# Optimization experiments

Measured on AMD Instinct MI355X. Metric: run time of the kernel, lower is better.

Reference implementation:

```python
import jax, jax.numpy as jnp
import numpy as np

N_NODES = 100000
N_EDGES = 3200000
IN_CH = 256
HIDDEN = 64
OUT_CH = 128


def setup_inputs() -> dict:
    key = jax.random.key(0)
    ks = jax.random.split(key, 6)
    x = jax.random.normal(ks[0], (N_NODES, IN_CH), dtype=jnp.float32)
    edge_index = jax.random.randint(ks[1], (2, N_EDGES), 0, N_NODES, dtype=jnp.int64)
    W1 = jax.random.normal(ks[2], (IN_CH, HIDDEN), dtype=jnp.float32) * (1.0 / np.sqrt(IN_CH))
    b1 = jnp.zeros((HIDDEN,), dtype=jnp.float32)
    W2 = jax.random.normal(ks[3], (HIDDEN, OUT_CH), dtype=jnp.float32) * (1.0 / np.sqrt(HIDDEN))
    b2 = jnp.zeros((OUT_CH,), dtype=jnp.float32)
    fcW = jax.random.normal(ks[4], (2, OUT_CH), dtype=jnp.float32) * (1.0 / np.sqrt(OUT_CH))
    fcb = jnp.zeros((2,), dtype=jnp.float32)
    return {"x": x, "edge_index": edge_index, "W1": W1, "b1": b1,
            "W2": W2, "b2": b2, "fcW": fcW, "fcb": fcb}


def _gcn_conv(x, edge_index, W, b):
    """PyG GCNConv: linear transform, add self-loops, symmetric D^-1/2 A D^-1/2 aggregation, bias."""
    N = x.shape[0]
    h = x @ W  # [N, F_out]
    loops = jnp.arange(N, dtype=edge_index.dtype)
    row = jnp.concatenate([edge_index[0], loops])  # source nodes
    col = jnp.concatenate([edge_index[1], loops])  # destination nodes
    deg = jax.ops.segment_sum(jnp.ones_like(col, dtype=h.dtype), col, num_segments=N)
    dinv = jnp.where(deg > 0, jax.lax.rsqrt(deg), 0.0)
    norm = dinv[row] * dinv[col]  # [E+N]
    out = jax.ops.segment_sum(h[row] * norm[:, None], col, num_segments=N)
    return out + b


def reference(x, edge_index, W1, b1, W2, b2, fcW, fcb):
    h = jax.nn.relu(_gcn_conv(x, edge_index, W1, b1))
    h = jax.nn.relu(_gcn_conv(h, edge_index, W2, b2))
    g = jnp.mean(h, axis=0)  # [OUT_CH]
    return g @ fcW.T + fcb   # [2]
```

## Files before the change

kernel.cpp:

```cpp
#include <hip/hip_runtime.h>

#define N_NODES 100000
#define N_EDGES 3200000
#define C_IN 256
#define C_H 64
#define C_OUT 128
#define NB 391
#define G2F 625
#define NTILES 6250
#define CH1 8192

typedef unsigned int u32;
typedef unsigned short u16;
typedef unsigned long long u64;
typedef __attribute__((ext_vector_type(8))) short bf16x8;
typedef __attribute__((ext_vector_type(4))) float f32x4;

__device__ __forceinline__ float bflo(u32 p) {
    union { u32 i; float f; } v; v.i = p << 16; return v.f;
}
__device__ __forceinline__ float bfhi(u32 p) {
    union { u32 i; float f; } v; v.i = p & 0xffff0000u; return v.f;
}
__device__ __forceinline__ float bf2f(u16 u) {
    union { u32 i; float f; } v; v.i = ((u32)u) << 16; return v.f;
}
__device__ __forceinline__ u16 f2bf(float f) {
    union { float f; u32 i; } v; v.f = f;
    u32 x = v.i;
    return (u16)((x + 0x7fffu + ((x >> 16) & 1u)) >> 16);
}

__global__ void k_detect(const void* __restrict__ x, const void* __restrict__ ei,
                         const void* __restrict__ b1, const void* __restrict__ b2,
                         const void* __restrict__ fcW, const void* __restrict__ fcb,
                         int* __restrict__ flags,
                         float* __restrict__ b1c, float* __restrict__ b2c,
                         float* __restrict__ fcWc, float* __restrict__ fcbc) {
    __shared__ int sf[2];
    int t = threadIdx.x;
    if (t < 64) {
        u32 w = ((const u32*)x)[t];
        u32 low = w & 0xffffu;
        int e = (int)((low >> 7) & 0xff);
        bool inw = (e > 96 && e < 160) || (low == 0);
        u64 m = __ballot(inw);
        if (t == 0) sf[0] = (__popcll(m) >= 60) ? 1 : 0;
    } else if (t < 128) {
        int i = t - 64;
        u32 w = ((const u32*)ei)[2 * i + 1];
        u64 m = __ballot(w == 0);
        if (i == 0) sf[1] = (m == ~0ull) ? 1 : 0;
    }
    __syncthreads();
    if (t == 0) { flags[0] = sf[0]; flags[1] = sf[1]; }
    int isbf = sf[0];
    if (isbf) {
        const u16* p1 = (const u16*)b1;  const u16* p2 = (const u16*)b2;
        const u16* pw = (const u16*)fcW; const u16* pb = (const u16*)fcb;
        for (int i = t; i < C_H; i += 256) b1c[i] = bf2f(p1[i]);
        for (int i = t; i < C_OUT; i += 256) b2c[i] = bf2f(p2[i]);
        for (int i = t; i < 2 * C_OUT; i += 256) fcWc[i] = bf2f(pw[i]);
        for (int i = t; i < 2; i += 256) fcbc[i] = bf2f(pb[i]);
    } else {
        const float* p1 = (const float*)b1;  const float* p2 = (const float*)b2;
        const float* pw = (const float*)fcW; const float* pb = (const float*)fcb;
        for (int i = t; i < C_H; i += 256) b1c[i] = p1[i];
        for (int i = t; i < C_OUT; i += 256) b2c[i] = p2[i];
        for (int i = t; i < 2 * C_OUT; i += 256) fcWc[i] = pw[i];
        for (int i = t; i < 2; i += 256) fcbc[i] = pb[i];
    }
}

__global__ __launch_bounds__(256) void k_prep(const void* __restrict__ W1,
                                              const void* __restrict__ W2,
                                              const int* __restrict__ flags,
                                              u16* __restrict__ W1m, u16* __restrict__ W2m,
                                              u32* __restrict__ bucket_cnt) {
    int b = blockIdx.x, t = threadIdx.x;
    int isbf = flags[0];
    int i = b * 256 + t;
    if (i < NB) bucket_cnt[i] = 0;
    if (i < C_IN * C_H) {
        const u16* w1b = (const u16*)W1; const float* w1f = (const float*)W1;
        int j = i & 7, lane = (i >> 3) & 63, nt = (i >> 9) & 3, k0 = i >> 11;
        int k = k0 * 32 + ((lane >> 4) & 3) * 8 + j;
        int n = nt * 16 + (lane & 15);
        W1m[i] = isbf ? w1b[k * C_H + n] : f2bf(w1f[k * C_H + n]);
    } else {
        int i2 = i - C_IN * C_H;
        const u16* w2b = (const u16*)W2; const float* w2f = (const float*)W2;
        int j = i2 & 7, lane = (i2 >> 3) & 63, nt = (i2 >> 9) & 7, k0 = (i2 >> 12) & 1;
        int k = k0 * 32 + ((lane >> 4) & 3) * 8 + j;
        int n = nt * 16 + (lane & 15);
        W2m[i2] = isbf ? w2b[k * C_OUT + n] : f2bf(w2f[k * C_OUT + n]);
    }
}

__global__ __launch_bounds__(256) void k_hist1(const int* __restrict__ ei,
                                               const int* __restrict__ flags,
                                               u32* __restrict__ bucket_cnt) {
    __shared__ u32 h[NB];
    int t = threadIdx.x;
    int is64 = flags[1];
    for (int i = t; i < NB; i += 256) h[i] = 0;
    __syncthreads();
    int e0 = blockIdx.x * CH1;
    int nv = min(CH1, N_EDGES - e0);
    for (int i = t; i < nv; i += 256) {
        int e = e0 + i;
        int d = is64 ? ei[2 * (N_EDGES + e)] : ei[N_EDGES + e];
        atomicAdd(&h[d >> 8], 1u);
    }
    __syncthreads();
    for (int i = t; i < NB; i += 256)
        if (h[i]) atomicAdd(&bucket_cnt[i], h[i]);
}

__global__ __launch_bounds__(512) void k_bscan(const u32* __restrict__ bucket_cnt,
                                               u32* __restrict__ bucket_base,
                                               u32* __restrict__ bucket_cursor,
                                               int* __restrict__ rowptr) {
    __shared__ u32 sm[512];
    int t = threadIdx.x;
    u32 v = (t < NB) ? bucket_cnt[t] : 0;
    sm[t] = v;
    __syncthreads();
    for (int off = 1; off < 512; off <<= 1) {
        u32 a = (t >= off) ? sm[t - off] : 0;
        __syncthreads();
        sm[t] += a;
        __syncthreads();
    }
    if (t < NB) {
        u32 excl = sm[t] - v;
        bucket_base[t] = excl;
        bucket_cursor[t] = excl;
    }
    if (t == 0) {
        bucket_base[NB] = N_EDGES;
        rowptr[N_NODES] = N_EDGES;
    }
}

__global__ __launch_bounds__(512) void k_scatter1(const int* __restrict__ ei,
                                                  const int* __restrict__ flags,
                                                  u32* __restrict__ bucket_cursor,
                                                  u32* __restrict__ ebuf) {
    __shared__ u32 cnt[NB];
    __shared__ u32 lcur[NB];
    __shared__ u32 gbase[NB];
    __shared__ u32 lofs[512];
    __shared__ u32 stp[CH1];
    __shared__ u16 stb[CH1];
    int t = threadIdx.x;
    int is64 = flags[1];
    int e0 = blockIdx.x * CH1;
    int nv = min(CH1, N_EDGES - e0);
    for (int i = t; i < NB; i += 512) { cnt[i] = 0; lcur[i] = 0; }
    __syncthreads();
    for (int i = t; i < nv; i += 512) {
        int e = e0 + i;
        int d = is64 ? ei[2 * (N_EDGES + e)] : ei[N_EDGES + e];
        atomicAdd(&cnt[d >> 8], 1u);
    }
    __syncthreads();
    u32 v = (t < NB) ? cnt[t] : 0;
    lofs[t] = v;
    __syncthreads();
    for (int off = 1; off < 512; off <<= 1) {
        u32 a = (t >= off) ? lofs[t - off] : 0;
        __syncthreads();
        lofs[t] += a;
        __syncthreads();
    }
    u32 excl = lofs[t] - v;
    __syncthreads();
    lofs[t] = excl;
    __syncthreads();
    for (int i = t; i < nv; i += 512) {
        int e = e0 + i;
        int d, s;
        if (is64) { d = ei[2 * (N_EDGES + e)]; s = ei[2 * e]; }
        else      { d = ei[N_EDGES + e];       s = ei[e]; }
        int b = d >> 8;
        u32 slot = lofs[b] + atomicAdd(&lcur[b], 1u);
        stp[slot] = ((u32)(d & 255) << 20) | (u32)s;
        stb[slot] = (u16)b;
    }
    __syncthreads();
    for (int b = t; b < NB; b += 512) {
        u32 c = cnt[b];
        gbase[b] = c ? atomicAdd(&bucket_cursor[b], c) : 0;
    }
    __syncthreads();
    for (int s = t; s < nv; s += 512) {
        int b = stb[s];
        ebuf[gbase[b] + (s - lofs[b])] = stp[s];
    }
}

__global__ __launch_bounds__(256) void k_scatter2(const u32* __restrict__ bucket_base,
                                                  const u32* __restrict__ ebuf,
                                                  int* __restrict__ rowptr,
                                                  float* __restrict__ dinv,
                                                  int* __restrict__ csr) {
    __shared__ int cnt[256];
    __shared__ int pfx[256];
    __shared__ int lcur[256];
    int b = blockIdx.x, t = threadIdx.x;
    int ebeg = (int)bucket_base[b], eend = (int)bucket_base[b + 1];
    cnt[t] = 0;
    lcur[t] = 0;
    __syncthreads();
    for (int i = ebeg + t; i < eend; i += 256)
        atomicAdd(&cnt[(ebuf[i] >> 20) & 255], 1);
    __syncthreads();
    int v = cnt[t];
    pfx[t] = v;
    __syncthreads();
    for (int off = 1; off < 256; off <<= 1) {
        int a = (t >= off) ? pfx[t - off] : 0;
        __syncthreads();
        pfx[t] += a;
        __syncthreads();
    }
    int node = (b << 8) + t;
    if (node < N_NODES) {
        rowptr[node] = ebeg + (pfx[t] - v);
        dinv[node] = rsqrtf((float)(v + 1));
    }
    __syncthreads();
    for (int i = ebeg + t; i < eend; i += 256) {
        u32 p = ebuf[i];
        int dl = (p >> 20) & 255;
        int pos = ebeg + (pfx[dl] - cnt[dl]) + atomicAdd(&lcur[dl], 1);
        csr[pos] = (int)(p & 0x1FFFFu);
    }
}

__global__ __launch_bounds__(256) void k_gemm1(const void* __restrict__ xv,
                                               const u16* __restrict__ W1m,
                                               const float* __restrict__ dinv,
                                               u16* __restrict__ g1,
                                               const int* __restrict__ flags) {
    __shared__ u16 wlds[C_IN * C_H];
    int t = threadIdx.x;
    int isbf = flags[0];
    {
        const uint4* src = (const uint4*)W1m;
        uint4* dst = (uint4*)wlds;
#pragma unroll
        for (int it = 0; it < 8; ++it) dst[t + it * 256] = src[t + it * 256];
    }
    __syncthreads();
    int w = t >> 6, lane = t & 63;
    int quad = lane >> 4, mrow = lane & 15;
    int m0 = blockIdx.x * 128 + w * 32;
    if (m0 >= N_NODES) return;

    bf16x8 a[2][8];
    if (isbf) {
        const u16* xb = (const u16*)xv;
#pragma unroll
        for (int mt = 0; mt < 2; ++mt)
#pragma unroll
            for (int k0 = 0; k0 < 8; ++k0)
                a[mt][k0] = *(const bf16x8*)(xb + (size_t)(m0 + mt * 16 + mrow) * C_IN + k0 * 32 + quad * 8);
    } else {
        const float* xf = (const float*)xv;
#pragma unroll
        for (int mt = 0; mt < 2; ++mt)
#pragma unroll
            for (int k0 = 0; k0 < 8; ++k0) {
                const float* p = xf + (size_t)(m0 + mt * 16 + mrow) * C_IN + k0 * 32 + quad * 8;
                float4 v0 = *(const float4*)p;
                float4 v1 = *(const float4*)(p + 4);
                bf16x8 r;
                r[0] = (short)f2bf(v0.x); r[1] = (short)f2bf(v0.y);
                r[2] = (short)f2bf(v0.z); r[3] = (short)f2bf(v0.w);
                r[4] = (short)f2bf(v1.x); r[5] = (short)f2bf(v1.y);
                r[6] = (short)f2bf(v1.z); r[7] = (short)f2bf(v1.w);
                a[mt][k0] = r;
            }
    }

    float dv0[4], dv1[4];
#pragma unroll
    for (int r = 0; r < 4; ++r) {
        dv0[r] = dinv[m0 + quad * 4 + r];
        dv1[r] = dinv[m0 + 16 + quad * 4 + r];
    }

#pragma unroll
    for (int nt = 0; nt < 4; ++nt) {
        bf16x8 b[8];
#pragma unroll
        for (int k0 = 0; k0 < 8; ++k0)
            b[k0] = *(const bf16x8*)&wlds[((k0 * 4 + nt) * 64 + lane) * 8];
        f32x4 acc0 = {0.f, 0.f, 0.f, 0.f};
        f32x4 acc1 = {0.f, 0.f, 0.f, 0.f};
#pragma unroll
        for (int k0 = 0; k0 < 8; ++k0) {
            acc0 = __builtin_amdgcn_mfma_f32_16x16x32_bf16(a[0][k0], b[k0], acc0, 0, 0, 0);
            acc1 = __builtin_amdgcn_mfma_f32_16x16x32_bf16(a[1][k0], b[k0], acc1, 0, 0, 0);
        }
        int ch = nt * 16 + mrow;
#pragma unroll
        for (int r = 0; r < 4; ++r) {
            g1[(size_t)(m0 + quad * 4 + r) * C_H + ch] = f2bf(acc0[r] * dv0[r]);
            g1[(size_t)(m0 + 16 + quad * 4 + r) * C_H + ch] = f2bf(acc1[r] * dv1[r]);
        }
    }
}

template <int MODE>
__global__ __launch_bounds__(256) void k_gatherT(const int* __restrict__ rowptr,
                                                 const int* __restrict__ csr_src,
                                                 const float* __restrict__ dinv,
                                                 const u16* __restrict__ g,
                                                 const float* __restrict__ bias,
                                                 u16* __restrict__ out) {
    int t = threadIdx.x;
    int w = t >> 6, lane = t & 63;
    int grp = lane >> 3, c = lane & 7;
    int n = blockIdx.x * 4 + w;
    int beg = rowptr[n], end = rowptr[n + 1];
    float acc[8] = {0.f, 0.f, 0.f, 0.f, 0.f, 0.f, 0.f, 0.f};
    int e = beg + grp;
    for (; e + 8 < end; e += 16) {
        int sa = csr_src[e];
        int sb = csr_src[e + 8];
        uint4 pa = *(const uint4*)(g + (size_t)sa * C_H + c * 8);
        uint4 pb = *(const uint4*)(g + (size_t)sb * C_H + c * 8);
        acc[0] += bflo(pa.x); acc[1] += bfhi(pa.x);
        acc[2] += bflo(pa.y); acc[3] += bfhi(pa.y);
        acc[4] += bflo(pa.z); acc[5] += bfhi(pa.z);
        acc[6] += bflo(pa.w); acc[7] += bfhi(pa.w);
        acc[0] += bflo(pb.x); acc[1] += bfhi(pb.x);
        acc[2] += bflo(pb.y); acc[3] += bfhi(pb.y);
        acc[4] += bflo(pb.z); acc[5] += bfhi(pb.z);
        acc[6] += bflo(pb.w); acc[7] += bfhi(pb.w);
    }
    if (e < end) {
        int sa = csr_src[e];
        uint4 pa = *(const uint4*)(g + (size_t)sa * C_H + c * 8);
        acc[0] += bflo(pa.x); acc[1] += bfhi(pa.x);
        acc[2] += bflo(pa.y); acc[3] += bfhi(pa.y);
        acc[4] += bflo(pa.z); acc[5] += bfhi(pa.z);
        acc[6] += bflo(pa.w); acc[7] += bfhi(pa.w);
    }
#pragma unroll
    for (int i = 0; i < 8; ++i) {
        acc[i] += __shfl_xor(acc[i], 8, 64);
        acc[i] += __shfl_xor(acc[i], 16, 64);
        acc[i] += __shfl_xor(acc[i], 32, 64);
    }
    if (grp == 0) {
        float dn = dinv[n];
        uint4 pn = *(const uint4*)(g + (size_t)n * C_H + c * 8);
        float sf[8];
        sf[0] = bflo(pn.x); sf[1] = bfhi(pn.x);
        sf[2] = bflo(pn.y); sf[3] = bfhi(pn.y);
        sf[4] = bflo(pn.z); sf[5] = bfhi(pn.z);
        sf[6] = bflo(pn.w); sf[7] = bfhi(pn.w);
        u32 res[4];
#pragma unroll
        for (int k = 0; k < 4; ++k) {
            float vA = dn * (acc[2 * k] + sf[2 * k]);
            float vB = dn * (acc[2 * k + 1] + sf[2 * k + 1]);
            if (MODE == 0) {
                vA = dn * fmaxf(vA + bias[c * 8 + 2 * k], 0.f);
                vB = dn * fmaxf(vB + bias[c * 8 + 2 * k + 1], 0.f);
            }
            res[k] = (u32)f2bf(vA) | ((u32)f2bf(vB) << 16);
        }
        uint4 pk;
        pk.x = res[0]; pk.y = res[1]; pk.z = res[2]; pk.w = res[3];
        *(uint4*)(out + (size_t)n * C_H + c * 8) = pk;
    }
}

__global__ __launch_bounds__(256) void k_fused2(const u16* __restrict__ aggb,
                                                const u16* __restrict__ W2m,
                                                const float* __restrict__ b2c,
                                                float* __restrict__ partial) {
    __shared__ float psum[4 * 8 * 64];
    int t = threadIdx.x;
    int w = t >> 6, lane = t & 63;
    int quad = lane >> 4, m = lane & 15;

    bf16x8 b[2][8];
#pragma unroll
    for (int k0 = 0; k0 < 2; ++k0)
#pragma unroll
        for (int nt = 0; nt < 8; ++nt)
            b[k0][nt] = *(const bf16x8*)&W2m[((k0 * 8 + nt) * 64 + lane) * 8];

    float pacc[8] = {0.f, 0.f, 0.f, 0.f, 0.f, 0.f, 0.f, 0.f};
    float bias[8];
#pragma unroll
    for (int nt = 0; nt < 8; ++nt) bias[nt] = b2c[nt * 16 + m];

    for (int tile = blockIdx.x * 4 + w; tile < NTILES; tile += G2F * 4) {
        const u16* arow = aggb + (size_t)(tile * 16 + m) * C_H + quad * 8;
        bf16x8 a0 = *(const bf16x8*)(arow);
        bf16x8 a1 = *(const bf16x8*)(arow + 32);
#pragma unroll
        for (int nt = 0; nt < 8; ++nt) {
            f32x4 acc = {0.f, 0.f, 0.f, 0.f};
            acc = __builtin_amdgcn_mfma_f32_16x16x32_bf16(a0, b[0][nt], acc, 0, 0, 0);
            acc = __builtin_amdgcn_mfma_f32_16x16x32_bf16(a1, b[1][nt], acc, 0, 0, 0);
#pragma unroll
            for (int r = 0; r < 4; ++r)
                pacc[nt] += fmaxf(acc[r] + bias[nt], 0.f);
        }
    }
#pragma unroll
    for (int nt = 0; nt < 8; ++nt) psum[(w * 8 + nt) * 64 + lane] = pacc[nt];
    __syncthreads();
    if (t < 128) {
        int nt = t >> 4, m2 = t & 15;
        float s = 0.f;
#pragma unroll
        for (int ww = 0; ww < 4; ++ww)
#pragma unroll
            for (int q = 0; q < 4; ++q)
                s += psum[(ww * 8 + nt) * 64 + q * 16 + m2];
        partial[blockIdx.x * C_OUT + t] = s;
    }
}

__global__ __launch_bounds__(512) void k_final(const float* __restrict__ partial,
                                               const float* __restrict__ fcWc,
                                               const float* __restrict__ fcbc,
                                               void* __restrict__ out,
                                               const int* __restrict__ flags) {
    __shared__ float sm[512];
    __shared__ float red[256];
    int t = threadIdx.x;
    int f = t & 127, c = t >> 7;
    float s = 0.f;
    for (int b = c; b < G2F; b += 4) s += partial[b * 128 + f];
    sm[t] = s;
    __syncthreads();
    if (t < 128) {
        float gm = (sm[t] + sm[t + 128] + sm[t + 256] + sm[t + 384]) * (1.0f / (float)N_NODES);
        red[t] = gm * fcWc[t];
        red[128 + t] = gm * fcWc[128 + t];
    }
    __syncthreads();
    for (int off = 64; off >= 1; off >>= 1) {
        if (t < off) {
            red[t] += red[t + off];
            red[128 + t] += red[128 + t + off];
        }
        __syncthreads();
    }
    if (t == 0) {
        float o0 = red[0] + fcbc[0];
        float o1 = red[128] + fcbc[1];
        if (flags[0]) {
            u16* ob = (u16*)out;
            ob[0] = f2bf(o0);
            ob[1] = f2bf(o1);
        } else {
            float* of = (float*)out;
            of[0] = o0;
            of[1] = o1;
        }
    }
}

#define OFF_FLAGS   0u
#define OFF_DINV    512u
#define OFF_ROWPTR  400896u
#define OFF_BCNT    801280u
#define OFF_BBASE   802944u
#define OFF_BCUR    804608u
#define OFF_CSR     1201664u
#define OFF_H1      14001664u
#define OFF_A1      26801664u
#define OFF_AGG     39601664u
#define OFF_PART    65201664u
#define OFF_W1C     65728000u
#define OFF_W2C     65760768u
#define OFF_B1C     65777152u
#define OFF_B2C     65777408u
#define OFF_FCWC    65777920u
#define OFF_FCBC    65778944u

extern "C" void kernel_launch(void* const* d_in, const int* in_sizes, int n_in,
                              void* d_out, int out_size, void* d_ws, size_t ws_size,
                              hipStream_t stream) {
    (void)in_sizes; (void)n_in; (void)out_size; (void)ws_size;
    const void* x   = d_in[0];
    const int*  ei  = (const int*)d_in[1];
    const void* W1  = d_in[2];
    const void* b1  = d_in[3];
    const void* W2  = d_in[4];
    const void* b2  = d_in[5];
    const void* fcW = d_in[6];
    const void* fcb = d_in[7];

    char* ws = (char*)d_ws;
    int*   flags  = (int*)(ws + OFF_FLAGS);
    float* dinv   = (float*)(ws + OFF_DINV);
    int*   rowptr = (int*)(ws + OFF_ROWPTR);
    u32*   bcnt   = (u32*)(ws + OFF_BCNT);
    u32*   bbase  = (u32*)(ws + OFF_BBASE);
    u32*   bcur   = (u32*)(ws + OFF_BCUR);
    int*   csr    = (int*)(ws + OFF_CSR);
    u16*   g1     = (u16*)(ws + OFF_H1);
    u16*   a1s    = (u16*)(ws + OFF_A1);
    u16*   aggb   = (u16*)(ws + OFF_AGG);
    u32*   ebuf   = (u32*)(ws + OFF_AGG);
    float* partial= (float*)(ws + OFF_PART);
    u16*   W1m    = (u16*)(ws + OFF_W1C);
    u16*   W2m    = (u16*)(ws + OFF_W2C);
    float* b1c    = (float*)(ws + OFF_B1C);
    float* b2c    = (float*)(ws + OFF_B2C);
    float* fcWc   = (float*)(ws + OFF_FCWC);
    float* fcbc   = (float*)(ws + OFF_FCBC);

    k_detect<<<1, 256, 0, stream>>>(x, ei, b1, b2, fcW, fcb,
                                    flags, b1c, b2c, fcWc, fcbc);
    k_prep<<<96, 256, 0, stream>>>(W1, W2, flags, W1m, W2m, bcnt);
    k_hist1<<<NB, 256, 0, stream>>>(ei, flags, bcnt);
    k_bscan<<<1, 512, 0, stream>>>(bcnt, bbase, bcur, rowptr);
    k_scatter1<<<NB, 512, 0, stream>>>(ei, flags, bcur, ebuf);
    k_scatter2<<<NB, 256, 0, stream>>>(bbase, ebuf, rowptr, dinv, csr);
    k_gemm1<<<(N_NODES + 127) / 128, 256, 0, stream>>>(x, W1m, dinv, g1, flags);
    k_gatherT<0><<<N_NODES / 4, 256, 0, stream>>>(rowptr, csr, dinv, g1, b1c, a1s);
    k_gatherT<1><<<N_NODES / 4, 256, 0, stream>>>(rowptr, csr, dinv, a1s, (const float*)nullptr, aggb);
    k_fused2<<<G2F, 256, 0, stream>>>(aggb, W2m, b2c, partial);
    k_final<<<1, 512, 0, stream>>>(partial, fcWc, fcbc, (void*)d_out, flags);
}
```

Baseline: 416.3 us.

## Rewrite neighbor gather as MFMA segment-sum with LDS async loads and inline self-loops

```diff
diff --git a/kernel.cpp b/kernel.cpp
--- a/kernel.cpp
+++ b/kernel.cpp
@@ -8,6 +8,8 @@
 #define NB 391
 #define G2F 625
 #define NTILES 6250
+#define NT16 6250
+#define G_GM 1563
 #define CH1 8192
 
 typedef unsigned int u32;
@@ -16,6 +18,9 @@
 typedef __attribute__((ext_vector_type(8))) short bf16x8;
 typedef __attribute__((ext_vector_type(4))) float f32x4;
 
+typedef __attribute__((address_space(3))) unsigned int l_u32;
+typedef __attribute__((address_space(1))) const unsigned int g_u32;
+
 __device__ __forceinline__ float bflo(u32 p) {
     union { u32 i; float f; } v; v.i = p << 16; return v.f;
 }
@@ -29,6 +34,10 @@
     union { float f; u32 i; } v; v.f = f;
     u32 x = v.i;
     return (u16)((x + 0x7fffu + ((x >> 16) & 1u)) >> 16);
+}
+
+__device__ __forceinline__ void gll16(const void* gp, const u16* lp) {
+    __builtin_amdgcn_global_load_lds((g_u32*)gp, (l_u32*)lp, 16, 0, 0);
 }
 
 __global__ void k_detect(const void* __restrict__ x, const void* __restrict__ ei,
@@ -137,10 +146,8 @@
         bucket_base[t] = excl;
         bucket_cursor[t] = excl;
     }
-    if (t == 0) {
-        bucket_base[NB] = N_EDGES;
-        rowptr[N_NODES] = N_EDGES;
-    }
+    if (t == 0) bucket_base[NB] = N_EDGES;
+    (void)rowptr;
 }
 
 __global__ __launch_bounds__(512) void k_scatter1(const int* __restrict__ ei,
@@ -210,6 +217,7 @@
     __shared__ int lcur[256];
     int b = blockIdx.x, t = threadIdx.x;
     int ebeg = (int)bucket_base[b], eend = (int)bucket_base[b + 1];
+    int sbeg = ebeg + (b << 8);
     cnt[t] = 0;
     lcur[t] = 0;
     __syncthreads();
@@ -226,16 +234,22 @@
         __syncthreads();
     }
     int node = (b << 8) + t;
+    int rstart = sbeg + (pfx[t] - v) + t;
     if (node < N_NODES) {
-        rowptr[node] = ebeg + (pfx[t] - v);
+        rowptr[node] = rstart;
         dinv[node] = rsqrtf((float)(v + 1));
+        csr[rstart] = node << 7;
+        if (node == N_NODES - 1) {
+            rowptr[N_NODES] = rstart + v + 1;
+            for (int i = 0; i < 64; ++i) csr[rstart + v + 1 + i] = 0;
+        }
     }
     __syncthreads();
     for (int i = ebeg + t; i < eend; i += 256) {
         u32 p = ebuf[i];
         int dl = (p >> 20) & 255;
-        int pos = ebeg + (pfx[dl] - cnt[dl]) + atomicAdd(&lcur[dl], 1);
-        csr[pos] = (int)(p & 0x1FFFFu);
+        int pos = sbeg + (pfx[dl] - cnt[dl]) + dl + 1 + atomicAdd(&lcur[dl], 1);
+        csr[pos] = (int)((p & 0x1FFFFu) << 7);
     }
 }
 
@@ -315,70 +329,109 @@
 }
 
 template <int MODE>
-__global__ __launch_bounds__(256) void k_gatherT(const int* __restrict__ rowptr,
-                                                 const int* __restrict__ csr_src,
+__global__ __launch_bounds__(256) void k_gatherM(const int* __restrict__ rowptr,
+                                                 const int* __restrict__ csrb,
                                                  const float* __restrict__ dinv,
-                                                 const u16* __restrict__ g,
+                                                 const u16* __restrict__ gt,
                                                  const float* __restrict__ bias,
                                                  u16* __restrict__ out) {
-    int t = threadIdx.x;
+    __shared__ __align__(16) u16 hs[4][4096];
+    __shared__ bf16x8 lut[81];
+    int t = threadIdx.x;
+    if (t < 81) {
+        int s = t / 9, e = t - s * 9;
+        bf16x8 le;
+#pragma unroll
+        for (int j = 0; j < 8; ++j) le[j] = (short)((j >= s && j < e) ? 0x3F80 : 0);
+        lut[t] = le;
+    }
+    __syncthreads();
     int w = t >> 6, lane = t & 63;
-    int grp = lane >> 3, c = lane & 7;
-    int n = blockIdx.x * 4 + w;
-    int beg = rowptr[n], end = rowptr[n + 1];
-    float acc[8] = {0.f, 0.f, 0.f, 0.f, 0.f, 0.f, 0.f, 0.f};
-    int e = beg + grp;
-    for (; e + 8 < end; e += 16) {
-        int sa = csr_src[e];
-        int sb = csr_src[e + 8];
-        uint4 pa = *(const uint4*)(g + (size_t)sa * C_H + c * 8);
-        uint4 pb = *(const uint4*)(g + (size_t)sb * C_H + c * 8);
-        acc[0] += bflo(pa.x); acc[1] += bfhi(pa.x);
-        acc[2] += bflo(pa.y); acc[3] += bfhi(pa.y);
-        acc[4] += bflo(pa.z); acc[5] += bfhi(pa.z);
-        acc[6] += bflo(pa.w); acc[7] += bfhi(pa.w);
-        acc[0] += bflo(pb.x); acc[1] += bfhi(pb.x);
-        acc[2] += bflo(pb.y); acc[3] += bfhi(pb.y);
-        acc[4] += bflo(pb.z); acc[5] += bfhi(pb.z);
-        acc[6] += bflo(pb.w); acc[7] += bfhi(pb.w);
-    }
-    if (e < end) {
-        int sa = csr_src[e];
-        uint4 pa = *(const uint4*)(g + (size_t)sa * C_H + c * 8);
-        acc[0] += bflo(pa.x); acc[1] += bfhi(pa.x);
-        acc[2] += bflo(pa.y); acc[3] += bfhi(pa.y);
-        acc[4] += bflo(pa.z); acc[5] += bfhi(pa.z);
-        acc[6] += bflo(pa.w); acc[7] += bfhi(pa.w);
-    }
-#pragma unroll
-    for (int i = 0; i < 8; ++i) {
-        acc[i] += __shfl_xor(acc[i], 8, 64);
-        acc[i] += __shfl_xor(acc[i], 16, 64);
-        acc[i] += __shfl_xor(acc[i], 32, 64);
-    }
-    if (grp == 0) {
-        float dn = dinv[n];
-        uint4 pn = *(const uint4*)(g + (size_t)n * C_H + c * 8);
-        float sf[8];
-        sf[0] = bflo(pn.x); sf[1] = bfhi(pn.x);
-        sf[2] = bflo(pn.y); sf[3] = bfhi(pn.y);
-        sf[4] = bflo(pn.z); sf[5] = bfhi(pn.z);
-        sf[6] = bflo(pn.w); sf[7] = bfhi(pn.w);
-        u32 res[4];
-#pragma unroll
-        for (int k = 0; k < 4; ++k) {
-            float vA = dn * (acc[2 * k] + sf[2 * k]);
-            float vB = dn * (acc[2 * k + 1] + sf[2 * k + 1]);
-            if (MODE == 0) {
-                vA = dn * fmaxf(vA + bias[c * 8 + 2 * k], 0.f);
-                vB = dn * fmaxf(vB + bias[c * 8 + 2 * k + 1], 0.f);
-            }
-            res[k] = (u32)f2bf(vA) | ((u32)f2bf(vB) << 16);
-        }
-        uint4 pk;
-        pk.x = res[0]; pk.y = res[1]; pk.z = res[2]; pk.w = res[3];
-        *(uint4*)(out + (size_t)n * C_H + c * 8) = pk;
-    }
+    int tile = blockIdx.x * 4 + w;
+    if (tile >= NT16) return;
+
+    int g16 = lane >> 4, c = lane & 15;
+    int n0 = tile << 4;
+    int lo = rowptr[n0 + c];
+    int hi = rowptr[n0 + c + 1];
+    int beg = __shfl(lo, 0, 64);
+    int end = __shfl(hi, 15, 64);
+    int eidx = lane >> 3;
+    int boff = (lane & 7) * 16;
+    const char* gb = (const char*)gt;
+    f32x4 acc0 = {0.f, 0.f, 0.f, 0.f}, acc1 = acc0, acc2 = acc0, acc3 = acc0;
+    int nch = (end - beg + 31) >> 5;
+    int cb = beg;
+    {
+        u32 o0 = (u32)csrb[cb + eidx];
+        u32 o1 = (u32)csrb[cb + 8 + eidx];
+        u32 o2 = (u32)csrb[cb + 16 + eidx];
+        u32 o3 = (u32)csrb[cb + 24 + eidx];
+        gll16(gb + o0 + boff, &hs[w][0]);
+        gll16(gb + o1 + boff, &hs[w][512]);
+        gll16(gb + o2 + boff, &hs[w][1024]);
+        gll16(gb + o3 + boff, &hs[w][1536]);
+        asm volatile("" ::: "memory");
+    }
+    for (int ci = 0; ci < nch; ++ci) {
+        int cbn = cb + 32;
+        bool more = (ci + 1 < nch);
+        u32 n0o = 0, n1o = 0, n2o = 0, n3o = 0;
+        if (more) {
+            n0o = (u32)csrb[cbn + eidx];
+            n1o = (u32)csrb[cbn + 8 + eidx];
+            n2o = (u32)csrb[cbn + 16 + eidx];
+            n3o = (u32)csrb[cbn + 24 + eidx];
+        }
+        if (more) asm volatile("s_waitcnt vmcnt(4)" ::: "memory");
+        else      asm volatile("s_waitcnt vmcnt(0)" ::: "memory");
+        const u16* lp = &hs[w][((ci & 1) << 11) + g16 * 512 + ((c >> 3) << 3) + (c & 7)];
+        bf16x8 bfr[4];
+#pragma unroll
+        for (int cht = 0; cht < 4; ++cht) {
+            u32 w0 = (u32)lp[0 * 64 + cht * 16] | ((u32)lp[1 * 64 + cht * 16] << 16);
+            u32 w1 = (u32)lp[2 * 64 + cht * 16] | ((u32)lp[3 * 64 + cht * 16] << 16);
+            u32 w2 = (u32)lp[4 * 64 + cht * 16] | ((u32)lp[5 * 64 + cht * 16] << 16);
+            u32 w3 = (u32)lp[6 * 64 + cht * 16] | ((u32)lp[7 * 64 + cht * 16] << 16);
+            union { u32 u[4]; bf16x8 v; } z;
+            z.u[0] = w0; z.u[1] = w1; z.u[2] = w2; z.u[3] = w3;
+            bfr[cht] = z.v;
+        }
+        int cbg = cb + g16 * 8;
+        int s0 = min(max(lo - cbg, 0), 8);
+        int e0 = min(max(hi - cbg, 0), 8);
+        bf16x8 af = lut[s0 * 9 + e0];
+        acc0 = __builtin_amdgcn_mfma_f32_16x16x32_bf16(af, bfr[0], acc0, 0, 0, 0);
+        acc1 = __builtin_amdgcn_mfma_f32_16x16x32_bf16(af, bfr[1], acc1, 0, 0, 0);
+        acc2 = __builtin_amdgcn_mfma_f32_16x16x32_bf16(af, bfr[2], acc2, 0, 0, 0);
+        acc3 = __builtin_amdgcn_mfma_f32_16x16x32_bf16(af, bfr[3], acc3, 0, 0, 0);
+        if (more) {
+            int bo = ((ci + 1) & 1) << 11;
+            gll16(gb + n0o + boff, &hs[w][bo]);
+            gll16(gb + n1o + boff, &hs[w][bo + 512]);
+            gll16(gb + n2o + boff, &hs[w][bo + 1024]);
+            gll16(gb + n3o + boff, &hs[w][bo + 1536]);
+            asm volatile("" ::: "memory");
+        }
+        cb = cbn;
+    }
+    float dv[4];
+    int nb = n0 + g16 * 4;
+#pragma unroll
+    for (int r = 0; r < 4; ++r) dv[r] = dinv[nb + r];
+    u16* ob = out + (size_t)nb * C_H + c;
+#define EPI(ACC, CHT)                                                              \
+    {                                                                              \
+        float bs = (MODE == 0) ? bias[CHT * 16 + c] : 0.f;                         \
+        _Pragma("unroll")                                                          \
+        for (int r = 0; r < 4; ++r) {                                              \
+            float val = (MODE == 0) ? dv[r] * fmaxf(dv[r] * ACC[r] + bs, 0.f)      \
+                                    : dv[r] * ACC[r];                              \
+            ob[r * C_H + CHT * 16] = f2bf(val);                                    \
+        }                                                                          \
+    }
+    EPI(acc0, 0) EPI(acc1, 1) EPI(acc2, 2) EPI(acc3, 3)
+#undef EPI
 }
 
 __global__ __launch_bounds__(256) void k_fused2(const u16* __restrict__ aggb,
@@ -479,16 +532,16 @@
 #define OFF_BBASE   802944u
 #define OFF_BCUR    804608u
 #define OFF_CSR     1201664u
-#define OFF_H1      14001664u
-#define OFF_A1      26801664u
-#define OFF_AGG     39601664u
-#define OFF_PART    65201664u
-#define OFF_W1C     65728000u
-#define OFF_W2C     65760768u
-#define OFF_B1C     65777152u
-#define OFF_B2C     65777408u
-#define OFF_FCWC    65777920u
-#define OFF_FCBC    65778944u
+#define OFF_H1      14402560u
+#define OFF_A1      27202560u
+#define OFF_AGG     40002560u
+#define OFF_PART    52802560u
+#define OFF_W1C     53122560u
+#define OFF_W2C     53155328u
+#define OFF_B1C     53171712u
+#define OFF_B2C     53171968u
+#define OFF_FCWC    53172480u
+#define OFF_FCBC    53173504u
 
 extern "C" void kernel_launch(void* const* d_in, const int* in_sizes, int n_in,
                               void* d_out, int out_size, void* d_ws, size_t ws_size,
@@ -531,8 +584,8 @@
     k_scatter1<<<NB, 512, 0, stream>>>(ei, flags, bcur, ebuf);
     k_scatter2<<<NB, 256, 0, stream>>>(bbase, ebuf, rowptr, dinv, csr);
     k_gemm1<<<(N_NODES + 127) / 128, 256, 0, stream>>>(x, W1m, dinv, g1, flags);
-    k_gatherT<0><<<N_NODES / 4, 256, 0, stream>>>(rowptr, csr, dinv, g1, b1c, a1s);
-    k_gatherT<1><<<N_NODES / 4, 256, 0, stream>>>(rowptr, csr, dinv, a1s, (const float*)nullptr, aggb);
+    k_gatherM<0><<<G_GM, 256, 0, stream>>>(rowptr, csr, dinv, g1, b1c, a1s);
+    k_gatherM<1><<<G_GM, 256, 0, stream>>>(rowptr, csr, dinv, a1s, b2c, aggb);
     k_fused2<<<G2F, 256, 0, stream>>>(aggb, W2m, b2c, partial);
     k_final<<<1, 512, 0, stream>>>(partial, fcWc, fcbc, (void*)d_out, flags);
 }
```

Result: faster. 401.4 us (-3.6%).
